# Performance work log

Hardware: AMD Instinct MI355X
Metric: run time of the kernel (lower is better)

Reference implementation:

```python
import jax, jax.numpy as jnp
import numpy as np

NHEAD = 16
FREQ = 10000.0


def rope(x, freq=FREQ):
    # x: [B, S, D]; rotary applied over the FULL feature dim (pre head-split),
    # pairing even/odd channels, matching the original module's op order.
    B, S, D = x.shape
    inv_freq = freq ** (-jnp.arange(0, D, 2, dtype=jnp.float32) / D)  # [D/2]
    ang = jnp.arange(S, dtype=jnp.float32)[:, None] * inv_freq[None, :]  # [S, D/2]
    cos, sin = jnp.cos(ang), jnp.sin(ang)
    x1, x2 = x[..., 0::2], x[..., 1::2]
    out_even = x1 * cos - x2 * sin
    out_odd = x1 * sin + x2 * cos
    return jnp.stack([out_even, out_odd], axis=-1).reshape(B, S, D)


def setup_inputs() -> dict:
    key = jax.random.key(0)
    ks = jax.random.split(key, 9)
    B, S, D = 4, 2048, 1024
    sc = 1.0 / np.sqrt(D)
    return {
        "queries": jax.random.normal(ks[0], (B, S, D), jnp.float32),
        "Wq": jax.random.normal(ks[1], (D, D), jnp.float32) * sc,
        "bq": jnp.zeros((D,), jnp.float32),
        "Wk": jax.random.normal(ks[2], (D, D), jnp.float32) * sc,
        "bk": jnp.zeros((D,), jnp.float32),
        "Wv": jax.random.normal(ks[3], (D, D), jnp.float32) * sc,
        "bv": jnp.zeros((D,), jnp.float32),
        "Wo": jax.random.normal(ks[4], (D, D), jnp.float32) * sc,
        "bo": jnp.zeros((D,), jnp.float32),
    }


def reference(queries, Wq, bq, Wk, bk, Wv, bv, Wo, bo):
    B, S, D = queries.shape
    H = NHEAD
    dh = D // H
    # self-attention: values = keys = queries
    q = rope(queries @ Wq.T + bq)
    k = rope(queries @ Wk.T + bk)
    v = queries @ Wv.T + bv
    # separate heads: [B, S, D] -> [B, H, S, dh]
    q = q.reshape(B, S, H, dh).transpose(0, 2, 1, 3)
    k = k.reshape(B, S, H, dh).transpose(0, 2, 1, 3)
    v = v.reshape(B, S, H, dh).transpose(0, 2, 1, 3)
    scores = jnp.einsum("bhqd,bhkd->bhqk", q, k) / jnp.sqrt(jnp.float32(dh))
    attn = jax.nn.softmax(scores, axis=-1)
    heads = jnp.einsum("bhqk,bhkd->bhqd", attn, v)
    out = heads.transpose(0, 2, 1, 3).reshape(B, S, D)
    return out @ Wo.T + bo
```

## Files before the change

kernel.cpp:

```cpp
#include <hip/hip_runtime.h>
#include <stdint.h>

typedef __bf16 bf16_t;
typedef __bf16 bf16x4 __attribute__((ext_vector_type(4)));
typedef __bf16 bf16x8 __attribute__((ext_vector_type(8)));
typedef float  f32x4  __attribute__((ext_vector_type(4)));

#define BB   4
#define SS   2048
#define DD   1024
#define HH   16
#define DH   64

#if __has_builtin(__builtin_amdgcn_exp2f)
#define EXP2F(x) __builtin_amdgcn_exp2f(x)
#else
#define EXP2F(x) __expf((x) * 0.6931471805599453f)
#endif

__device__ __forceinline__ void gload_lds16(const void* g, void* l) {
    __builtin_amdgcn_global_load_lds(
        (__attribute__((address_space(1))) void*)(uintptr_t)g,
        (__attribute__((address_space(3))) void*)(uint32_t)(uintptr_t)l,
        16, 0, 0);
}

__global__ __launch_bounds__(256) void prep_kernel(
        const float* __restrict__ queries,
        const float* __restrict__ Wq, const float* __restrict__ Wk,
        const float* __restrict__ Wv, const float* __restrict__ Wo,
        const float* __restrict__ bq, const float* __restrict__ bk,
        const float* __restrict__ bv,
        bf16_t* __restrict__ Xb, bf16_t* __restrict__ Wqkv,
        bf16_t* __restrict__ Wob, float* __restrict__ bqkv,
        float2* __restrict__ tab)
{
    const int bid = blockIdx.x, t = threadIdx.x;
    if (bid < 8192) {
        const int i = bid * 256 + t;
        float4 v = ((const float4*)queries)[i];
        bf16x4 o;
        o.x = (bf16_t)v.x; o.y = (bf16_t)v.y; o.z = (bf16_t)v.z; o.w = (bf16_t)v.w;
        ((bf16x4*)Xb)[i] = o;
    } else if (bid < 12288) {
        const int i = (bid - 8192) * 256 + t;
        const int which = i >> 18, p = i & 262143;
        const float* src = (which == 0) ? Wq : (which == 1) ? Wk : (which == 2) ? Wv : Wo;
        bf16_t* dst = (which < 3) ? (Wqkv + (long)which * 1048576) : Wob;
        float4 v = ((const float4*)src)[p];
        bf16x4 o;
        o.x = (bf16_t)v.x; o.y = (bf16_t)v.y; o.z = (bf16_t)v.z; o.w = (bf16_t)v.w;
        ((bf16x4*)dst)[p] = o;
    } else if (bid < 16384) {
        const int i = (bid - 12288) * 256 + t;
        const int s = i >> 9, pr = i & 511;
        float inv = powf(10000.0f, -(float)(2 * pr) * (1.0f / 1024.0f));
        float c, sn;
        sincosf((float)s * inv, &sn, &c);
        tab[i] = make_float2(c, sn);
    } else {
        const int i = (bid - 16384) * 256 + t;
        if (i < 3072)
            bqkv[i] = (i < 1024) ? bq[i] : ((i < 2048) ? bk[i - 1024] : bv[i - 2048]);
    }
}

__global__ __launch_bounds__(256, 3) void gemm_qkv_rope(
        const bf16_t* __restrict__ A, const bf16_t* __restrict__ Bm,
        const float* __restrict__ bias, const float2* __restrict__ tab,
        bf16_t* __restrict__ Qb, bf16_t* __restrict__ Kb, bf16_t* __restrict__ Vt)
{
    __shared__ __attribute__((aligned(16))) bf16_t As[128 * 32];
    __shared__ __attribute__((aligned(16))) bf16_t Bs[128 * 32];
    const int t = threadIdx.x;
    const int lane = t & 63, w = t >> 6;
    const int wm = w >> 1, wn = w & 1;
    const int l15 = lane & 15, l4 = lane >> 4;
    const int xg = l15 & 3;
    const long rowA0 = (long)blockIdx.x * 128;
    const long rowB0 = (long)blockIdx.y * 128;
    const int K = 1024;

    const f32x4 vz = {0.f, 0.f, 0.f, 0.f};
    f32x4 acc[4][4];
#pragma unroll
    for (int i = 0; i < 4; ++i)
#pragma unroll
        for (int j = 0; j < 4; ++j) acc[i][j] = vz;

    for (int kk = 0; kk < K; kk += 32) {
        __syncthreads();
#pragma unroll
        for (int i = 0; i < 2; ++i) {
            const int cb = i * 256 + w * 64;
            const int c  = cb + lane;
            const int r  = c >> 2;
            const int ko = ((c & 3) ^ (r & 3)) << 3;
            gload_lds16(A  + (rowA0 + r) * K + kk + ko, As + cb * 8);
            gload_lds16(Bm + (rowB0 + r) * K + kk + ko, Bs + cb * 8);
        }
        __syncthreads();
        bf16x8 af[4], bfr[4];
#pragma unroll
        for (int i = 0; i < 4; ++i)
            af[i] = *(const bf16x8*)(As + (wm * 64 + i * 16 + l15) * 32 + ((l4 ^ xg) * 8));
#pragma unroll
        for (int j = 0; j < 4; ++j)
            bfr[j] = *(const bf16x8*)(Bs + (wn * 64 + j * 16 + l15) * 32 + ((l4 ^ xg) * 8));
#pragma unroll
        for (int i = 0; i < 4; ++i)
#pragma unroll
            for (int j = 0; j < 4; ++j)
                acc[i][j] = __builtin_amdgcn_mfma_f32_16x16x32_bf16(af[i], bfr[j], acc[i][j], 0, 0, 0);
    }

    const long crow0 = rowA0 + wm * 64;
    const int  ccol0 = (int)rowB0 + wn * 64;
    const int  part  = blockIdx.y >> 3;
    const int  b     = (int)(crow0 >> 11);
    const int  s0    = (int)(crow0 & 2047);

    if (part == 2) {
        const int h = (ccol0 - 2048) >> 6;
#pragma unroll
        for (int j = 0; j < 4; ++j) {
            const int d = j * 16 + l15;
            const float bb = bias[ccol0 + j * 16 + l15];
            bf16_t* dstc = Vt + ((long)(b * HH + h) * DH + d) * SS + s0;
#pragma unroll
            for (int i = 0; i < 4; ++i) {
                bf16x4 pk;
                pk.x = (bf16_t)(acc[i][j][0] + bb);
                pk.y = (bf16_t)(acc[i][j][1] + bb);
                pk.z = (bf16_t)(acc[i][j][2] + bb);
                pk.w = (bf16_t)(acc[i][j][3] + bb);
                *(bf16x4*)(dstc + i * 16 + l4 * 4) = pk;
            }
        }
    } else {
        bf16_t* dst0 = part ? Kb : Qb;
        const int h = (ccol0 & 1023) >> 6;
        const int even = !(l15 & 1);
#pragma unroll
        for (int i = 0; i < 4; ++i) {
#pragma unroll
            for (int j = 0; j < 4; ++j) {
                const int col = ccol0 + j * 16 + l15;
                const float bb = bias[col];
                const int dd = j * 16 + l15;
                const float2* trow = tab + (col >> 1 & 511);
#pragma unroll
                for (int r = 0; r < 4; ++r) {
                    const int s = s0 + i * 16 + l4 * 4 + r;
                    const float val = acc[i][j][r] + bb;
                    const float par = __shfl_xor(val, 1);
                    const float2 cs = trow[s * 512];
                    const float out = even ? (val * cs.x - par * cs.y)
                                           : fmaf(val, cs.x, par * cs.y);
                    const float op = __shfl_xor(out, 1);
                    if (even) {
                        union { bf16_t hh[2]; unsigned int u; } cv;
                        cv.hh[0] = (bf16_t)out; cv.hh[1] = (bf16_t)op;
                        *(unsigned int*)(dst0 + ((long)((b * HH + h) * SS + s)) * DH + dd) = cv.u;
                    }
                }
            }
        }
    }
}

template <int OUT_BF16>
__global__ __launch_bounds__(256, 3) void gemm_bt(
        const bf16_t* __restrict__ A, const bf16_t* __restrict__ Bm,
        const float* __restrict__ bias, void* __restrict__ Cout,
        int M, int N, int K)
{
    __shared__ __attribute__((aligned(16))) bf16_t As[128 * 32];
    __shared__ __attribute__((aligned(16))) bf16_t Bs[128 * 32];
    const int t = threadIdx.x;
    const int lane = t & 63, w = t >> 6;
    const int wm = w >> 1, wn = w & 1;
    const int l15 = lane & 15, l4 = lane >> 4;
    const int xg = l15 & 3;
    const long rowA0 = (long)blockIdx.x * 128;
    const long rowB0 = (long)blockIdx.y * 128;

    const f32x4 vz = {0.f, 0.f, 0.f, 0.f};
    f32x4 acc[4][4];
#pragma unroll
    for (int i = 0; i < 4; ++i)
#pragma unroll
        for (int j = 0; j < 4; ++j) acc[i][j] = vz;

    for (int kk = 0; kk < K; kk += 32) {
        __syncthreads();
#pragma unroll
        for (int i = 0; i < 2; ++i) {
            const int cb = i * 256 + w * 64;
            const int c  = cb + lane;
            const int r  = c >> 2;
            const int ko = ((c & 3) ^ (r & 3)) << 3;
            gload_lds16(A  + (rowA0 + r) * K + kk + ko, As + cb * 8);
            gload_lds16(Bm + (rowB0 + r) * K + kk + ko, Bs + cb * 8);
        }
        __syncthreads();
        bf16x8 af[4], bfr[4];
#pragma unroll
        for (int i = 0; i < 4; ++i)
            af[i] = *(const bf16x8*)(As + (wm * 64 + i * 16 + l15) * 32 + ((l4 ^ xg) * 8));
#pragma unroll
        for (int j = 0; j < 4; ++j)
            bfr[j] = *(const bf16x8*)(Bs + (wn * 64 + j * 16 + l15) * 32 + ((l4 ^ xg) * 8));
#pragma unroll
        for (int i = 0; i < 4; ++i)
#pragma unroll
            for (int j = 0; j < 4; ++j)
                acc[i][j] = __builtin_amdgcn_mfma_f32_16x16x32_bf16(af[i], bfr[j], acc[i][j], 0, 0, 0);
    }

    const long crow0 = rowA0 + wm * 64;
    const int  ccol0 = (int)rowB0 + wn * 64;
#pragma unroll
    for (int i = 0; i < 4; ++i) {
#pragma unroll
        for (int j = 0; j < 4; ++j) {
            const int col = ccol0 + j * 16 + l15;
            const float bb = bias[col];
#pragma unroll
            for (int r = 0; r < 4; ++r) {
                const long row = crow0 + i * 16 + l4 * 4 + r;
                const float v = acc[i][j][r] + bb;
                if (OUT_BF16) ((bf16_t*)Cout)[row * N + col] = (bf16_t)v;
                else          ((float*)Cout)[row * N + col]  = v;
            }
        }
    }
}

__global__ __launch_bounds__(256, 4) void attn_kernel(const bf16_t* __restrict__ Qb,
                                                      const bf16_t* __restrict__ Kb,
                                                      const bf16_t* __restrict__ Vt,
                                                      bf16_t* __restrict__ Ob)
{
    __shared__ __attribute__((aligned(16))) bf16_t Ks[64 * 64];
    __shared__ __attribute__((aligned(16))) bf16_t Vs[64 * 64];
    __shared__ __attribute__((aligned(16))) bf16_t Ps[128 * 72];
    const int t = threadIdx.x, lane = t & 63, w = t >> 6;
    const int l15 = lane & 15, l4 = lane >> 4;
    const int xr = l15 & 7;
    const int qt = blockIdx.x, bh = blockIdx.y;
    const bf16_t* Qbh = Qb + (long)bh * SS * DH;
    const bf16_t* Kbh = Kb + (long)bh * SS * DH;
    const bf16_t* Vbh = Vt + (long)bh * DH * SS;

    const int qbase = qt * 128 + w * 32;
    bf16x8 qf[2][2];
#pragma unroll
    for (int s = 0; s < 2; ++s) {
        const long qrow = qbase + 16 * s + l15;
        qf[s][0] = *(const bf16x8*)(Qbh + qrow * DH + l4 * 8);
        qf[s][1] = *(const bf16x8*)(Qbh + qrow * DH + 32 + l4 * 8);
    }

    const f32x4 vz = {0.f, 0.f, 0.f, 0.f};
    f32x4 oacc[2][4];
#pragma unroll
    for (int s = 0; s < 2; ++s)
#pragma unroll
        for (int j = 0; j < 4; ++j) oacc[s][j] = vz;
    float l_sum[2] = {0.f, 0.f};

    int srow[2], scc[2];
#pragma unroll
    for (int i = 0; i < 2; ++i) {
        const int L = i * 256 + w * 64 + lane;
        srow[i] = L >> 3;
        scc[i]  = (L & 7) ^ (srow[i] & 7);
    }

    const float SC = 0.125f * 1.4426950408889634f;
    const float BI = -8.0f  * 1.4426950408889634f;

    for (int kt = 0; kt < SS / 64; ++kt) {
        __syncthreads();
        const bf16_t* Ksrc = Kbh + (long)kt * 64 * DH;
#pragma unroll
        for (int i = 0; i < 2; ++i) {
            const int cb = i * 256 + w * 64;
            gload_lds16(Ksrc + srow[i] * 64 + scc[i] * 8, Ks + cb * 8);
            gload_lds16(Vbh + (long)srow[i] * SS + kt * 64 + scc[i] * 8, Vs + cb * 8);
        }
        __syncthreads();

        f32x4 sacc[2][4];
#pragma unroll
        for (int s = 0; s < 2; ++s)
#pragma unroll
            for (int j = 0; j < 4; ++j) sacc[s][j] = vz;
#pragma unroll
        for (int j = 0; j < 4; ++j) {
            const int rk = (j * 16 + l15) * 64;
            const bf16x8 kf0 = *(const bf16x8*)(Ks + rk + ((l4 ^ xr) * 8));
            const bf16x8 kf1 = *(const bf16x8*)(Ks + rk + (((4 + l4) ^ xr) * 8));
#pragma unroll
            for (int s = 0; s < 2; ++s) {
                sacc[s][j] = __builtin_amdgcn_mfma_f32_16x16x32_bf16(kf0, qf[s][0], sacc[s][j], 0, 0, 0);
                sacc[s][j] = __builtin_amdgcn_mfma_f32_16x16x32_bf16(kf1, qf[s][1], sacc[s][j], 0, 0, 0);
            }
        }

#pragma unroll
        for (int s = 0; s < 2; ++s) {
#pragma unroll
            for (int j = 0; j < 4; ++j) {
                const float p0 = EXP2F(fmaf(sacc[s][j][0], SC, BI));
                const float p1 = EXP2F(fmaf(sacc[s][j][1], SC, BI));
                const float p2 = EXP2F(fmaf(sacc[s][j][2], SC, BI));
                const float p3 = EXP2F(fmaf(sacc[s][j][3], SC, BI));
                l_sum[s] += (p0 + p1) + (p2 + p3);
                bf16x4 pk;
                pk.x = (bf16_t)p0; pk.y = (bf16_t)p1; pk.z = (bf16_t)p2; pk.w = (bf16_t)p3;
                *(bf16x4*)(Ps + (w * 32 + 16 * s + l15) * 72 + j * 16 + l4 * 4) = pk;
            }
        }

        bf16x8 pf[2][2];
#pragma unroll
        for (int s = 0; s < 2; ++s) {
            pf[s][0] = *(const bf16x8*)(Ps + (w * 32 + 16 * s + l15) * 72 + l4 * 8);
            pf[s][1] = *(const bf16x8*)(Ps + (w * 32 + 16 * s + l15) * 72 + 32 + l4 * 8);
        }
#pragma unroll
        for (int j = 0; j < 4; ++j) {
            const int rv = (j * 16 + l15) * 64;
            const bf16x8 vf0 = *(const bf16x8*)(Vs + rv + ((l4 ^ xr) * 8));
            const bf16x8 vf1 = *(const bf16x8*)(Vs + rv + (((4 + l4) ^ xr) * 8));
#pragma unroll
            for (int s = 0; s < 2; ++s) {
                oacc[s][j] = __builtin_amdgcn_mfma_f32_16x16x32_bf16(pf[s][0], vf0, oacc[s][j], 0, 0, 0);
                oacc[s][j] = __builtin_amdgcn_mfma_f32_16x16x32_bf16(pf[s][1], vf1, oacc[s][j], 0, 0, 0);
            }
        }
    }

    const int b = bh >> 4, h = bh & 15;
#pragma unroll
    for (int s = 0; s < 2; ++s) {
        float lt = l_sum[s];
        lt += __shfl_xor(lt, 16);
        lt += __shfl_xor(lt, 32);
        const float inv = 1.0f / lt;
        float invr[4];
#pragma unroll
        for (int r = 0; r < 4; ++r)
            invr[r] = __shfl(inv, l4 * 4 + r);
#pragma unroll
        for (int j = 0; j < 4; ++j) {
#pragma unroll
            for (int r = 0; r < 4; ++r) {
                const int row = qbase + 16 * s + l4 * 4 + r;
                const float v = oacc[s][j][r] * invr[r];
                Ob[((long)(b * SS + row)) * DD + h * DH + j * 16 + l15] = (bf16_t)v;
            }
        }
    }
}

extern "C" void kernel_launch(void* const* d_in, const int* in_sizes, int n_in,
                              void* d_out, int out_size, void* d_ws, size_t ws_size,
                              hipStream_t stream)
{
    const float* queries = (const float*)d_in[0];
    const float* Wq = (const float*)d_in[1];
    const float* bq = (const float*)d_in[2];
    const float* Wk = (const float*)d_in[3];
    const float* bk = (const float*)d_in[4];
    const float* Wv = (const float*)d_in[5];
    const float* bv = (const float*)d_in[6];
    const float* Wo = (const float*)d_in[7];
    const float* bo = (const float*)d_in[8];

    char* ws = (char*)d_ws;
    size_t off = 0;
    auto alloc = [&](size_t bytes) { size_t o = off; off += (bytes + 255) & ~(size_t)255; return o; };
    bf16_t* Xb   = (bf16_t*)(ws + alloc(8192u * 1024u * 2u));
    bf16_t* Wqkv = (bf16_t*)(ws + alloc(3072u * 1024u * 2u));
    bf16_t* Wob  = (bf16_t*)(ws + alloc(1024u * 1024u * 2u));
    float*  bqkv = (float*) (ws + alloc(3072u * 4u));
    float2* tab  = (float2*)(ws + alloc(2048u * 512u * 8u));
    bf16_t* Qb   = (bf16_t*)(ws + alloc(64u * 2048u * 64u * 2u));
    bf16_t* Kb   = (bf16_t*)(ws + alloc(64u * 2048u * 64u * 2u));
    bf16_t* Vt   = (bf16_t*)(ws + alloc(64u * 64u * 2048u * 2u));
    bf16_t* Ob   = Xb;

    prep_kernel<<<16396, 256, 0, stream>>>(queries, Wq, Wk, Wv, Wo, bq, bk, bv,
                                           Xb, Wqkv, Wob, bqkv, tab);

    gemm_qkv_rope<<<dim3(64, 24), 256, 0, stream>>>(Xb, Wqkv, bqkv, tab, Qb, Kb, Vt);
    attn_kernel<<<dim3(16, 64), 256, 0, stream>>>(Qb, Kb, Vt, Ob);
    gemm_bt<0><<<dim3(64, 8), 256, 0, stream>>>(Ob, Wob, bo, d_out, 8192, 1024, 1024);
}
```

Before: 294.2 us.

## Double-buffer K/V tiles and keep P in registers for PV MFMA

The attention kernel now double-buffers the K and V tiles in LDS and prefetches the next tile with async global-to-LDS loads while the current one is computed, using explicit vmcnt waits and barriers. The probability tile no longer round-trips through shared memory. The PV product uses 16x16x16 MFMAs fed directly from the score accumulator layout. The grid is also swapped so consecutive blocks share a batch-head for better K/V cache reuse. This trades extra MFMA instruction count and more LDS for the K/V buffers against removing the Ps LDS traffic and exposed load latency.

Measured after the change: 304.4 us. 1.03x slower.

```diff
diff --git a/kernel.cpp b/kernel.cpp
--- a/kernel.cpp
+++ b/kernel.cpp
@@ -5,6 +5,7 @@
 typedef __bf16 bf16x4 __attribute__((ext_vector_type(4)));
 typedef __bf16 bf16x8 __attribute__((ext_vector_type(8)));
 typedef float  f32x4  __attribute__((ext_vector_type(4)));
+typedef short  short4v __attribute__((ext_vector_type(4)));
 
 #define BB   4
 #define SS   2048
@@ -23,6 +24,15 @@
         (__attribute__((address_space(1))) void*)(uintptr_t)g,
         (__attribute__((address_space(3))) void*)(uint32_t)(uintptr_t)l,
         16, 0, 0);
+}
+
+__device__ __forceinline__ f32x4 mfma16(short4v a, short4v b, f32x4 c) {
+#if __has_builtin(__builtin_amdgcn_mfma_f32_16x16x16bf16_1k)
+    return __builtin_amdgcn_mfma_f32_16x16x16bf16_1k(a, b, c, 0, 0, 0);
+#else
+    asm("v_mfma_f32_16x16x16_bf16 %0, %1, %2, %0" : "+v"(c) : "v"(a), "v"(b));
+    return c;
+#endif
 }
 
 __global__ __launch_bounds__(256) void prep_kernel(
@@ -242,13 +252,12 @@
                                                       const bf16_t* __restrict__ Vt,
                                                       bf16_t* __restrict__ Ob)
 {
-    __shared__ __attribute__((aligned(16))) bf16_t Ks[64 * 64];
-    __shared__ __attribute__((aligned(16))) bf16_t Vs[64 * 64];
-    __shared__ __attribute__((aligned(16))) bf16_t Ps[128 * 72];
+    __shared__ __attribute__((aligned(16))) bf16_t Ks[2 * 64 * 64];
+    __shared__ __attribute__((aligned(16))) bf16_t Vs[2 * 64 * 64];
     const int t = threadIdx.x, lane = t & 63, w = t >> 6;
     const int l15 = lane & 15, l4 = lane >> 4;
     const int xr = l15 & 7;
-    const int qt = blockIdx.x, bh = blockIdx.y;
+    const int bh = blockIdx.x, qt = blockIdx.y;
     const bf16_t* Qbh = Qb + (long)bh * SS * DH;
     const bf16_t* Kbh = Kb + (long)bh * SS * DH;
     const bf16_t* Vbh = Vt + (long)bh * DH * SS;
@@ -261,6 +270,8 @@
         qf[s][0] = *(const bf16x8*)(Qbh + qrow * DH + l4 * 8);
         qf[s][1] = *(const bf16x8*)(Qbh + qrow * DH + 32 + l4 * 8);
     }
+    asm volatile("s_waitcnt vmcnt(0)" ::: "memory");
+    __builtin_amdgcn_sched_barrier(0);
 
     const f32x4 vz = {0.f, 0.f, 0.f, 0.f};
     f32x4 oacc[2][4];
@@ -280,17 +291,35 @@
 
     const float SC = 0.125f * 1.4426950408889634f;
     const float BI = -8.0f  * 1.4426950408889634f;
-
-    for (int kt = 0; kt < SS / 64; ++kt) {
-        __syncthreads();
-        const bf16_t* Ksrc = Kbh + (long)kt * 64 * DH;
+    const int NT = SS / 64;
+
+    auto stage = [&](int b, int kt2) {
+        const bf16_t* Ksrc = Kbh + (long)kt2 * 64 * DH;
 #pragma unroll
         for (int i = 0; i < 2; ++i) {
             const int cb = i * 256 + w * 64;
-            gload_lds16(Ksrc + srow[i] * 64 + scc[i] * 8, Ks + cb * 8);
-            gload_lds16(Vbh + (long)srow[i] * SS + kt * 64 + scc[i] * 8, Vs + cb * 8);
-        }
-        __syncthreads();
+            gload_lds16(Ksrc + srow[i] * 64 + scc[i] * 8, Ks + b * 4096 + cb * 8);
+            gload_lds16(Vbh + (long)srow[i] * SS + kt2 * 64 + scc[i] * 8, Vs + b * 4096 + cb * 8);
+        }
+    };
+
+    stage(0, 0);
+
+    for (int kt = 0; kt < NT; ++kt) {
+        const int cur = kt & 1;
+        if (kt + 1 < NT) {
+            stage(cur ^ 1, kt + 1);
+            __builtin_amdgcn_sched_barrier(0);
+            asm volatile("s_waitcnt vmcnt(4)" ::: "memory");
+        } else {
+            asm volatile("s_waitcnt vmcnt(0)" ::: "memory");
+        }
+        __builtin_amdgcn_sched_barrier(0);
+        __builtin_amdgcn_s_barrier();
+        __builtin_amdgcn_sched_barrier(0);
+
+        const bf16_t* Ksb = Ks + cur * 4096;
+        const bf16_t* Vsb = Vs + cur * 4096;
 
         f32x4 sacc[2][4];
 #pragma unroll
@@ -300,8 +329,8 @@
 #pragma unroll
         for (int j = 0; j < 4; ++j) {
             const int rk = (j * 16 + l15) * 64;
-            const bf16x8 kf0 = *(const bf16x8*)(Ks + rk + ((l4 ^ xr) * 8));
-            const bf16x8 kf1 = *(const bf16x8*)(Ks + rk + (((4 + l4) ^ xr) * 8));
+            const bf16x8 kf0 = *(const bf16x8*)(Ksb + rk + ((l4 ^ xr) * 8));
+            const bf16x8 kf1 = *(const bf16x8*)(Ksb + rk + (((4 + l4) ^ xr) * 8));
 #pragma unroll
             for (int s = 0; s < 2; ++s) {
                 sacc[s][j] = __builtin_amdgcn_mfma_f32_16x16x32_bf16(kf0, qf[s][0], sacc[s][j], 0, 0, 0);
@@ -309,6 +338,7 @@
             }
         }
 
+        short4v pf[2][4];
 #pragma unroll
         for (int s = 0; s < 2; ++s) {
 #pragma unroll
@@ -318,29 +348,27 @@
                 const float p2 = EXP2F(fmaf(sacc[s][j][2], SC, BI));
                 const float p3 = EXP2F(fmaf(sacc[s][j][3], SC, BI));
                 l_sum[s] += (p0 + p1) + (p2 + p3);
-                bf16x4 pk;
-                pk.x = (bf16_t)p0; pk.y = (bf16_t)p1; pk.z = (bf16_t)p2; pk.w = (bf16_t)p3;
-                *(bf16x4*)(Ps + (w * 32 + 16 * s + l15) * 72 + j * 16 + l4 * 4) = pk;
-            }
-        }
-
-        bf16x8 pf[2][2];
-#pragma unroll
-        for (int s = 0; s < 2; ++s) {
-            pf[s][0] = *(const bf16x8*)(Ps + (w * 32 + 16 * s + l15) * 72 + l4 * 8);
-            pf[s][1] = *(const bf16x8*)(Ps + (w * 32 + 16 * s + l15) * 72 + 32 + l4 * 8);
-        }
-#pragma unroll
-        for (int j = 0; j < 4; ++j) {
-            const int rv = (j * 16 + l15) * 64;
-            const bf16x8 vf0 = *(const bf16x8*)(Vs + rv + ((l4 ^ xr) * 8));
-            const bf16x8 vf1 = *(const bf16x8*)(Vs + rv + (((4 + l4) ^ xr) * 8));
-#pragma unroll
-            for (int s = 0; s < 2; ++s) {
-                oacc[s][j] = __builtin_amdgcn_mfma_f32_16x16x32_bf16(pf[s][0], vf0, oacc[s][j], 0, 0, 0);
-                oacc[s][j] = __builtin_amdgcn_mfma_f32_16x16x32_bf16(pf[s][1], vf1, oacc[s][j], 0, 0, 0);
-            }
-        }
+                union { bf16x4 h; short4v sv; } cv;
+                cv.h.x = (bf16_t)p0; cv.h.y = (bf16_t)p1;
+                cv.h.z = (bf16_t)p2; cv.h.w = (bf16_t)p3;
+                pf[s][j] = cv.sv;
+            }
+        }
+
+#pragma unroll
+        for (int dj = 0; dj < 4; ++dj) {
+            const bf16_t* vb = Vsb + (dj * 16 + l15) * 64 + (l4 & 1) * 4;
+#pragma unroll
+            for (int kb = 0; kb < 4; ++kb) {
+                const int slot = (kb * 2 + (l4 >> 1)) ^ xr;
+                const short4v vfr = *(const short4v*)(vb + slot * 8);
+                oacc[0][dj] = mfma16(pf[0][kb], vfr, oacc[0][dj]);
+                oacc[1][dj] = mfma16(pf[1][kb], vfr, oacc[1][dj]);
+            }
+        }
+
+        __builtin_amdgcn_sched_barrier(0);
+        __builtin_amdgcn_s_barrier();
     }
 
     const int b = bh >> 4, h = bh & 15;
@@ -397,6 +425,6 @@
                                            Xb, Wqkv, Wob, bqkv, tab);
 
     gemm_qkv_rope<<<dim3(64, 24), 256, 0, stream>>>(Xb, Wqkv, bqkv, tab, Qb, Kb, Vt);
-    attn_kernel<<<dim3(16, 64), 256, 0, stream>>>(Qb, Kb, Vt, Ob);
+    attn_kernel<<<dim3(64, 16), 256, 0, stream>>>(Qb, Kb, Vt, Ob);
     gemm_bt<0><<<dim3(64, 8), 256, 0, stream>>>(Ob, Wob, bo, d_out, 8192, 1024, 1024);
 }
```
